# Optimization experiments

Hardware: AMD Instinct MI355X
Metric: run time of the kernel (lower is better)

Reference implementation:

```python
import math
import jax, jax.numpy as jnp
import numpy as np

B, Q, L, H = 32, 40, 1024, 1024
WINDOW_FRAMES, MAX_V_L = 16, 1024
MAX_DELTA = 0.1
NUM_PASSES = 2


def setup_inputs() -> dict:
    key = jax.random.key(0)
    ks = jax.random.split(key, 8)
    init_log_sigma = math.log(WINDOW_FRAMES / (2.0 * MAX_V_L))
    return {
        "pred_spans": jax.random.uniform(ks[0], (B, Q, 2), dtype=jnp.float32),
        "vid_feat": jax.random.normal(ks[1], (B, L, H), dtype=jnp.float32),
        "vid_mask": jnp.ones((B, L), dtype=jnp.float32),
        "txt_rep": jax.random.normal(ks[2], (B, H), dtype=jnp.float32),
        "log_sigma_start": jnp.float32(init_log_sigma),
        "log_sigma_end": jnp.float32(init_log_sigma),
        "sigma_width_scale_start": jnp.float32(0.01),
        "sigma_width_scale_end": jnp.float32(-0.01),
        "txt_proj_w": jax.random.normal(ks[3], (H, 2), dtype=jnp.float32) * 0.02,
        "txt_proj_b": jnp.zeros((2,), dtype=jnp.float32),
        "mlp0_w": jax.random.normal(ks[4], (3 * H, H), dtype=jnp.float32) * (1.0 / math.sqrt(3 * H)),
        "mlp0_b": jnp.zeros((H,), dtype=jnp.float32),
        "mlp1_w": jax.random.normal(ks[5], (H, 2), dtype=jnp.float32) * (1.0 / math.sqrt(H)),
        "mlp1_b": jnp.zeros((2,), dtype=jnp.float32),
    }


def reference(pred_spans, vid_feat, vid_mask, txt_rep,
              log_sigma_start, log_sigma_end,
              sigma_width_scale_start, sigma_width_scale_end,
              txt_proj_w, txt_proj_b, mlp0_w, mlp0_b, mlp1_w, mlp1_b):
    b, q, _ = pred_spans.shape
    l = vid_feat.shape[1]
    # span (center,width) -> (start,end) in [0,1]
    start = jnp.clip(pred_spans[..., 0] - pred_spans[..., 1] / 2, 0.0, 1.0)  # (B,Q)
    end = jnp.clip(pred_spans[..., 0] + pred_spans[..., 1] / 2, 0.0, 1.0)
    t_pos = jnp.linspace(0.0, 1.0, l)  # (L,)
    min_sig = 1.0 / (4.0 * l)
    log_range = math.log(max(float(l) * min_sig * 4.0, 1.0 + 1e-6))
    # semantic sigma offsets (B,2)
    txt_off = jnp.tanh(txt_rep @ txt_proj_w + txt_proj_b) * (0.5 * log_range)
    txt_off_s, txt_off_e = txt_off[:, 0:1], txt_off[:, 1:2]  # (B,1)
    txt_expand = jnp.broadcast_to(txt_rep[:, None, :], (b, q, txt_rep.shape[-1]))
    mask = vid_mask[:, None, :]  # (B,1,L)

    def _pool(anchor, sigma):
        # Gaussian soft-attention pooling over frames; anchor,sigma: (B,Q)
        dist2 = ((t_pos[None, None, :] - anchor[:, :, None]) / sigma[:, :, None]) ** 2
        w = jnp.exp(-0.5 * dist2) * mask  # (B,Q,L)
        w = w / jnp.maximum(jnp.sum(w, -1, keepdims=True), 1e-8)
        return jnp.einsum('bql,blh->bqh', w, vid_feat)

    passes = []
    for _ in range(NUM_PASSES):
        width = jnp.maximum(end - start, 1e-6)  # (B,Q)
        sig_s = jnp.maximum(jnp.exp(log_sigma_start + sigma_width_scale_start * width + txt_off_s), min_sig)
        sig_e = jnp.maximum(jnp.exp(log_sigma_end + sigma_width_scale_end * width + txt_off_e), min_sig)
        start_feat = _pool(start, sig_s)
        end_feat = _pool(end, sig_e)
        joint = jnp.concatenate([start_feat, end_feat, txt_expand], axis=-1)  # (B,Q,3H)
        hidden = jax.nn.relu(joint @ mlp0_w + mlp0_b)
        deltas = jnp.tanh(hidden @ mlp1_w + mlp1_b) * MAX_DELTA  # (B,Q,2)
        start = jnp.clip(start + deltas[..., 0], 0.0, 1.0)
        end = jnp.clip(end + deltas[..., 1], 0.0, 1.0)
        center_r = (start + end) / 2.0
        width_r = jnp.maximum(end - start, 1e-6)
        passes.append(jnp.stack([center_r, width_r], axis=-1))
    return passes[-1], jnp.stack(passes, axis=0)
```

## Files before the change

kernel.cpp:

```cpp
#include <hip/hip_runtime.h>

#define B_   32
#define Q_   40
#define L_   1024
#define H_   1024
#define QQ_  80
#define M_   1280
#define K3_  3072
#define JK_  2048

#define OB_W0T   0u
#define OB_WT2   6291456u
#define OB_JOINT 11534336u
#define OB_PART  16777216u
#define OB_TXTB  27262976u
#define OB_TXTP  27328512u
#define OB_MISC  27590656u
#define MS_START 0
#define MS_END   1280
#define MS_TOS   2560
#define MS_TOE   2592

typedef short bf8 __attribute__((ext_vector_type(8)));
typedef float f4  __attribute__((ext_vector_type(4)));

static __device__ __forceinline__ unsigned short f2b(float f) {
    unsigned int x = __float_as_uint(f);
    unsigned int r = x + 0x7FFFu + ((x >> 16) & 1u);
    return (unsigned short)(r >> 16);
}
static __device__ __forceinline__ float b2f16(unsigned short u) {
    return __uint_as_float((unsigned int)u << 16);
}
static __device__ __forceinline__ float blo(unsigned int u) {
    return __uint_as_float(u << 16);
}
static __device__ __forceinline__ float bhi(unsigned int u) {
    return __uint_as_float(u & 0xffff0000u);
}

__global__ __launch_bounds__(256) void k_setup(const float* __restrict__ w0,
                                               unsigned short* __restrict__ w0t,
                                               const float* __restrict__ txt,
                                               const float* __restrict__ pw,
                                               const float* __restrict__ pb,
                                               const float* __restrict__ spans,
                                               unsigned short* __restrict__ txtb,
                                               float* __restrict__ msc) {
    int z = blockIdx.z, tid = threadIdx.x;
    if (z == 3) {
        int flat = blockIdx.x * 16 + blockIdx.y;
        if (flat < B_) {
            int b = flat;
            int h4 = tid * 4;
            float4 tv = *(const float4*)(txt + (size_t)b * H_ + h4);
            float4 pa = *(const float4*)(pw + 2 * h4);
            float4 pc = *(const float4*)(pw + 2 * h4 + 4);
            float s0 = tv.x * pa.x + tv.y * pa.z + tv.z * pc.x + tv.w * pc.z;
            float s1 = tv.x * pa.y + tv.y * pa.w + tv.z * pc.y + tv.w * pc.w;
            ushort4 o;
            o.x = f2b(tv.x); o.y = f2b(tv.y); o.z = f2b(tv.z); o.w = f2b(tv.w);
            *(ushort4*)(txtb + (size_t)b * H_ + h4) = o;
            __shared__ float r0[256], r1[256];
            r0[tid] = s0; r1[tid] = s1; __syncthreads();
            for (int off = 128; off > 0; off >>= 1) {
                if (tid < off) { r0[tid] += r0[tid + off]; r1[tid] += r1[tid + off]; }
                __syncthreads();
            }
            if (tid == 0) {
                const float half_lr = 4.9999975e-07f;
                msc[MS_TOS + b] = tanhf(r0[0] + pb[0]) * half_lr;
                msc[MS_TOE + b] = tanhf(r1[0] + pb[1]) * half_lr;
            }
        } else if (flat < 37) {
            int i = (flat - B_) * 256 + tid;
            if (i < M_) {
                float c = spans[2 * i], w = spans[2 * i + 1];
                msc[MS_START + i] = fminf(fmaxf(c - 0.5f * w, 0.f), 1.f);
                msc[MS_END + i]   = fminf(fmaxf(c + 0.5f * w, 0.f), 1.f);
            }
        }
        return;
    }
    __shared__ float tile[64][69];
    const float* s = w0 + (size_t)z * 1024 * H_;
    unsigned short* d = w0t + (size_t)z * 1024;
    int r0 = blockIdx.x * 64, c0 = blockIdx.y * 64;
    int col4 = (tid & 15) * 4, row = tid >> 4;
    #pragma unroll
    for (int it = 0; it < 4; it++) {
        int r = it * 16 + row;
        float4 v = *(const float4*)(s + (size_t)(r0 + r) * 1024 + c0 + col4);
        *(float4*)(&tile[r][col4]) = v;
    }
    __syncthreads();
    #pragma unroll
    for (int it = 0; it < 2; it++) {
        int slot = it * 256 + tid;
        int c = slot >> 3, chunk = slot & 7;
        int r = chunk * 8;
        uint4 vv;
        vv.x = (unsigned int)f2b(tile[r + 0][c]) | ((unsigned int)f2b(tile[r + 1][c]) << 16);
        vv.y = (unsigned int)f2b(tile[r + 2][c]) | ((unsigned int)f2b(tile[r + 3][c]) << 16);
        vv.z = (unsigned int)f2b(tile[r + 4][c]) | ((unsigned int)f2b(tile[r + 5][c]) << 16);
        vv.w = (unsigned int)f2b(tile[r + 6][c]) | ((unsigned int)f2b(tile[r + 7][c]) << 16);
        *(uint4*)(d + (size_t)(c0 + c) * K3_ + r0 + r) = vv;
    }
}

static __device__ __forceinline__ void weights_body(int m, float s, float e,
                                                    const float* __restrict__ vmask,
                                                    float ls_s, float ls_e,
                                                    float sw_s, float sw_e,
                                                    const float* __restrict__ msc,
                                                    unsigned short* __restrict__ wt2,
                                                    float* r0, float* r1) {
    int b = m / Q_, q = m - b * Q_;
    int tid = threadIdx.x;
    float width = fmaxf(e - s, 1e-6f);
    const float min_sig = 1.0f / (4.0f * (float)L_);
    float sig_s = fmaxf(expf(ls_s + sw_s * width + msc[MS_TOS + b]), min_sig);
    float sig_e = fmaxf(expf(ls_e + sw_e * width + msc[MS_TOE + b]), min_sig);
    float inv_s = 1.0f / sig_s, inv_e = 1.0f / sig_e;

    float wsv[4], wev[4], sumS = 0.f, sumE = 0.f;
    #pragma unroll
    for (int k = 0; k < 4; k++) {
        int l = tid + k * 256;
        float t = (float)l * (1.0f / 1023.0f);
        float mk = vmask[b * L_ + l];
        float ds = (t - s) * inv_s, de = (t - e) * inv_e;
        float a = expf(-0.5f * ds * ds) * mk;
        float c = expf(-0.5f * de * de) * mk;
        wsv[k] = a; wev[k] = c; sumS += a; sumE += c;
    }
    r0[tid] = sumS; r1[tid] = sumE; __syncthreads();
    for (int off = 128; off > 0; off >>= 1) {
        if (tid < off) { r0[tid] += r0[tid + off]; r1[tid] += r1[tid + off]; }
        __syncthreads();
    }
    float iS = 1.0f / fmaxf(r0[0], 1e-8f);
    float iE = 1.0f / fmaxf(r1[0], 1e-8f);
    unsigned short* wq = wt2 + ((size_t)b * QQ_ + q) * L_;
    unsigned short* we = wt2 + ((size_t)b * QQ_ + Q_ + q) * L_;
    #pragma unroll
    for (int k = 0; k < 4; k++) {
        int l = tid + k * 256;
        wq[l] = f2b(wsv[k] * iS);
        we[l] = f2b(wev[k] * iE);
    }
}

__global__ __launch_bounds__(256) void k_stage2(const float* __restrict__ vmask,
                                                const float* __restrict__ p_ls_s,
                                                const float* __restrict__ p_ls_e,
                                                const float* __restrict__ p_sw_s,
                                                const float* __restrict__ p_sw_e,
                                                const float* __restrict__ msc,
                                                unsigned short* __restrict__ wt2,
                                                const unsigned short* __restrict__ txtb,
                                                const unsigned short* __restrict__ w0t,
                                                unsigned short* __restrict__ txtp) {
    int bid = blockIdx.x;
    if (bid < M_) {
        __shared__ float r0[256], r1[256];
        int m = bid;
        weights_body(m, msc[MS_START + m], msc[MS_END + m], vmask,
                     p_ls_s[0], p_ls_e[0], p_sw_s[0], p_sw_e[0], msc, wt2, r0, r1);
        return;
    }
    int t = bid - M_;
    int nIdx = t & 15, mIdx = (t >> 4) & 1, kIdx = t >> 5;
    int wv = threadIdx.x >> 6, lane = threadIdx.x & 63;
    int ml = lane & 15, kg = lane >> 4;
    int mbase = mIdx * 16;
    int nbase = nIdx * 64 + wv * 16;
    int kz = kIdx * 256;
    const unsigned short* ap = txtb + ((size_t)(mbase + ml) * H_ + kz + kg * 8);
    const unsigned short* bp = w0t + ((size_t)(nbase + ml) * K3_ + JK_ + kz + kg * 8);
    f4 acc = (f4){0.f, 0.f, 0.f, 0.f};
    #pragma unroll
    for (int k0 = 0; k0 < 256; k0 += 32) {
        bf8 a = *(const bf8*)(ap + k0);
        bf8 bb = *(const bf8*)(bp + k0);
        acc = __builtin_amdgcn_mfma_f32_16x16x32_bf16(a, bb, acc, 0, 0, 0);
    }
    unsigned short* pp = txtp + (size_t)kIdx * B_ * H_;
    int n = nbase + ml;
    #pragma unroll
    for (int r = 0; r < 4; r++) {
        int m = mbase + kg * 4 + r;
        pp[(size_t)m * H_ + n] = f2b(acc[r]);
    }
}

__global__ __launch_bounds__(512) void k_pool_mfma(const float* __restrict__ vid,
                                                   const unsigned short* __restrict__ wt2,
                                                   unsigned short* __restrict__ joint) {
    int b = blockIdx.x, ht = blockIdx.y;
    int tid = threadIdx.x;
    int wv = tid >> 6, lane = tid & 63;
    int hsub = wv & 3, half = wv >> 2;
    int ml = lane & 15, kg = lane >> 4;
    int h0 = ht * 64;

    __shared__ __align__(16) unsigned short tileT[2][2][64][40];
    __shared__ float cmb[80][68];

    int st = tid & 255;
    int sl = st >> 3;
    int sh8 = (st & 7) * 8;
    const float* vbase = vid + ((size_t)b * L_ + half * 512) * H_ + h0;

    const unsigned short* ap = wt2 + ((size_t)b * QQ_ + ml) * L_ + half * 512 + kg * 8;

    f4 acc[5];
    #pragma unroll
    for (int t = 0; t < 5; t++) acc[t] = (f4){0.f, 0.f, 0.f, 0.f};

    {
        const float* src = vbase + (size_t)sl * H_ + sh8;
        float4 v0 = *(const float4*)(src);
        float4 v1 = *(const float4*)(src + 4);
        unsigned short* dst = &tileT[half][0][0][0];
        dst[(sh8 + 0) * 40 + sl] = f2b(v0.x);
        dst[(sh8 + 1) * 40 + sl] = f2b(v0.y);
        dst[(sh8 + 2) * 40 + sl] = f2b(v0.z);
        dst[(sh8 + 3) * 40 + sl] = f2b(v0.w);
        dst[(sh8 + 4) * 40 + sl] = f2b(v1.x);
        dst[(sh8 + 5) * 40 + sl] = f2b(v1.y);
        dst[(sh8 + 6) * 40 + sl] = f2b(v1.z);
        dst[(sh8 + 7) * 40 + sl] = f2b(v1.w);
    }
    __syncthreads();

    for (int c = 0; c < 16; c++) {
        int buf = c & 1;
        if (c < 15) {
            const float* src = vbase + (size_t)((c + 1) * 32 + sl) * H_ + sh8;
            float4 v0 = *(const float4*)(src);
            float4 v1 = *(const float4*)(src + 4);
            unsigned short* dst = &tileT[half][buf ^ 1][0][0];
            dst[(sh8 + 0) * 40 + sl] = f2b(v0.x);
            dst[(sh8 + 1) * 40 + sl] = f2b(v0.y);
            dst[(sh8 + 2) * 40 + sl] = f2b(v0.z);
            dst[(sh8 + 3) * 40 + sl] = f2b(v0.w);
            dst[(sh8 + 4) * 40 + sl] = f2b(v1.x);
            dst[(sh8 + 5) * 40 + sl] = f2b(v1.y);
            dst[(sh8 + 6) * 40 + sl] = f2b(v1.z);
            dst[(sh8 + 7) * 40 + sl] = f2b(v1.w);
        }
        bf8 bfrag = *(const bf8*)(&tileT[half][buf][hsub * 16 + ml][kg * 8]);
        int l0 = c * 32;
        #pragma unroll
        for (int t = 0; t < 5; t++) {
            bf8 afr = *(const bf8*)(ap + (size_t)t * 16 * L_ + l0);
            acc[t] = __builtin_amdgcn_mfma_f32_16x16x32_bf16(afr, bfrag, acc[t], 0, 0, 0);
        }
        __syncthreads();
    }

    if (half == 1) {
        #pragma unroll
        for (int t = 0; t < 5; t++)
            #pragma unroll
            for (int r = 0; r < 4; r++)
                cmb[t * 16 + kg * 4 + r][hsub * 16 + ml] = acc[t][r];
    }
    __syncthreads();
    if (half == 0) {
        #pragma unroll
        for (int t = 0; t < 5; t++)
            #pragma unroll
            for (int r = 0; r < 4; r++)
                cmb[t * 16 + kg * 4 + r][hsub * 16 + ml] += acc[t][r];
    }
    __syncthreads();
    for (int idx = tid; idx < 640; idx += 512) {
        int qq = idx >> 3, h8 = (idx & 7) * 8;
        const float* cr = &cmb[qq][h8];
        uint4 vv;
        vv.x = (unsigned int)f2b(cr[0]) | ((unsigned int)f2b(cr[1]) << 16);
        vv.y = (unsigned int)f2b(cr[2]) | ((unsigned int)f2b(cr[3]) << 16);
        vv.z = (unsigned int)f2b(cr[4]) | ((unsigned int)f2b(cr[5]) << 16);
        vv.w = (unsigned int)f2b(cr[6]) | ((unsigned int)f2b(cr[7]) << 16);
        int row = b * Q_ + (qq >= Q_ ? qq - Q_ : qq);
        int col = (qq >= Q_ ? H_ : 0) + h0 + h8;
        *(uint4*)(joint + (size_t)row * JK_ + col) = vv;
    }
}

__global__ __launch_bounds__(256) void k_mlp0_mfma(const unsigned short* __restrict__ joint,
                                                   const unsigned short* __restrict__ w0t,
                                                   const unsigned short* __restrict__ txtp,
                                                   unsigned short* __restrict__ part) {
    int wv = threadIdx.x >> 6, lane = threadIdx.x & 63;
    int ml = lane & 15, kg = lane >> 4;
    int mbase = blockIdx.x * 64 + wv * 16;
    int nbase = blockIdx.y * 64;
    int kbase = blockIdx.z * 512;
    const unsigned short* ap = joint + ((size_t)(mbase + ml) * JK_ + kbase + kg * 8);
    const unsigned short* bp = w0t + ((size_t)(nbase + ml) * K3_ + kbase + kg * 8);
    f4 acc[4];
    #pragma unroll
    for (int t = 0; t < 4; t++) acc[t] = (f4){0.f, 0.f, 0.f, 0.f};

    #pragma unroll 4
    for (int k0 = 0; k0 < 512; k0 += 32) {
        bf8 a = *(const bf8*)(ap + k0);
        #pragma unroll
        for (int t = 0; t < 4; t++) {
            bf8 bb = *(const bf8*)(bp + (size_t)t * 16 * K3_ + k0);
            acc[t] = __builtin_amdgcn_mfma_f32_16x16x32_bf16(a, bb, acc[t], 0, 0, 0);
        }
    }
    const unsigned short* tp = txtp + (size_t)blockIdx.z * B_ * H_;
    unsigned short* pp = part + (size_t)blockIdx.z * M_ * H_;
    #pragma unroll
    for (int t = 0; t < 4; t++) {
        int n = nbase + t * 16 + ml;
        #pragma unroll
        for (int r = 0; r < 4; r++) {
            int m = mbase + kg * 4 + r;
            int b = m / Q_;
            float v = acc[t][r] + b2f16(tp[(size_t)b * H_ + n]);
            pp[(size_t)m * H_ + n] = f2b(v);
        }
    }
}

__global__ __launch_bounds__(256) void k_mlp1w(const float* __restrict__ w1,
                                               const float* __restrict__ b0,
                                               const float* __restrict__ b1,
                                               const unsigned short* __restrict__ part,
                                               float* __restrict__ msc,
                                               float* __restrict__ out, int pass,
                                               int do_weights,
                                               const float* __restrict__ vmask,
                                               const float* __restrict__ p_ls_s,
                                               const float* __restrict__ p_ls_e,
                                               const float* __restrict__ p_sw_s,
                                               const float* __restrict__ p_sw_e,
                                               unsigned short* __restrict__ wt2) {
    int m = blockIdx.x, tid = threadIdx.x;
    int k4 = tid * 4;
    float4 bb = *(const float4*)(b0 + k4);
    float h0 = bb.x, h1 = bb.y, h2 = bb.z, h3 = bb.w;
    #pragma unroll
    for (int z = 0; z < 4; z++) {
        uint2 u = *(const uint2*)(part + (size_t)z * M_ * H_ + (size_t)m * H_ + k4);
        h0 += blo(u.x); h1 += bhi(u.x);
        h2 += blo(u.y); h3 += bhi(u.y);
    }
    h0 = fmaxf(h0, 0.f); h1 = fmaxf(h1, 0.f);
    h2 = fmaxf(h2, 0.f); h3 = fmaxf(h3, 0.f);
    float4 wa = *(const float4*)(w1 + 2 * k4);
    float4 wb = *(const float4*)(w1 + 2 * k4 + 4);
    float p0 = h0 * wa.x + h1 * wa.z + h2 * wb.x + h3 * wb.z;
    float p1 = h0 * wa.y + h1 * wa.w + h2 * wb.y + h3 * wb.w;

    __shared__ float r0[256], r1[256];
    __shared__ float sh_s, sh_e;
    r0[tid] = p0; r1[tid] = p1; __syncthreads();
    for (int off = 128; off > 0; off >>= 1) {
        if (tid < off) { r0[tid] += r0[tid + off]; r1[tid] += r1[tid + off]; }
        __syncthreads();
    }
    if (tid == 0) {
        float d0 = tanhf(r0[0] + b1[0]) * 0.1f;
        float d1 = tanhf(r1[0] + b1[1]) * 0.1f;
        float s = fminf(fmaxf(msc[MS_START + m] + d0, 0.f), 1.f);
        float e = fminf(fmaxf(msc[MS_END + m] + d1, 0.f), 1.f);
        msc[MS_START + m] = s;
        msc[MS_END + m] = e;
        sh_s = s; sh_e = e;
        float cen = 0.5f * (s + e);
        float wid = fmaxf(e - s, 1e-6f);
        out[2560 + (size_t)(pass * M_ + m) * 2 + 0] = cen;
        out[2560 + (size_t)(pass * M_ + m) * 2 + 1] = wid;
        if (pass == 1) { out[2 * m + 0] = cen; out[2 * m + 1] = wid; }
    }
    __syncthreads();
    if (do_weights) {
        weights_body(m, sh_s, sh_e, vmask,
                     p_ls_s[0], p_ls_e[0], p_sw_s[0], p_sw_e[0], msc, wt2, r0, r1);
    }
}

extern "C" void kernel_launch(void* const* d_in, const int* in_sizes, int n_in,
                              void* d_out, int out_size, void* d_ws, size_t ws_size,
                              hipStream_t stream) {
    const float* spans = (const float*)d_in[0];
    const float* vid   = (const float*)d_in[1];
    const float* vmask = (const float*)d_in[2];
    const float* txt   = (const float*)d_in[3];
    const float* ls_s  = (const float*)d_in[4];
    const float* ls_e  = (const float*)d_in[5];
    const float* sw_s  = (const float*)d_in[6];
    const float* sw_e  = (const float*)d_in[7];
    const float* pw    = (const float*)d_in[8];
    const float* pb    = (const float*)d_in[9];
    const float* w0    = (const float*)d_in[10];
    const float* b0    = (const float*)d_in[11];
    const float* w1    = (const float*)d_in[12];
    const float* b1    = (const float*)d_in[13];
    char* wsb = (char*)d_ws;
    unsigned short* w0t   = (unsigned short*)(wsb + OB_W0T);
    unsigned short* wt2   = (unsigned short*)(wsb + OB_WT2);
    unsigned short* joint = (unsigned short*)(wsb + OB_JOINT);
    unsigned short* part  = (unsigned short*)(wsb + OB_PART);
    unsigned short* txtb  = (unsigned short*)(wsb + OB_TXTB);
    unsigned short* txtp  = (unsigned short*)(wsb + OB_TXTP);
    float* msc = (float*)(wsb + OB_MISC);
    float* out = (float*)d_out;

    hipLaunchKernelGGL(k_setup, dim3(16, 16, 4), dim3(256), 0, stream,
                       w0, w0t, txt, pw, pb, spans, txtb, msc);
    hipLaunchKernelGGL(k_stage2, dim3(M_ + 128), dim3(256), 0, stream,
                       vmask, ls_s, ls_e, sw_s, sw_e, msc, wt2, txtb, w0t, txtp);
    for (int p = 0; p < 2; p++) {
        hipLaunchKernelGGL(k_pool_mfma, dim3(B_, 16), dim3(512), 0, stream, vid, wt2, joint);
        hipLaunchKernelGGL(k_mlp0_mfma, dim3(20, 16, 4), dim3(256), 0, stream,
                           joint, w0t, txtp, part);
        hipLaunchKernelGGL(k_mlp1w, dim3(M_), dim3(256), 0, stream,
                           w1, b0, b1, part, msc, out, p, (p == 0) ? 1 : 0,
                           vmask, ls_s, ls_e, sw_s, sw_e, wt2);
    }
}
```

Before: 395.8 us.

## Pre-transpose video features to bf16 once and simplify pooling MFMA kernel

Result: slower. 431.4 us (+9.0%).

```diff
diff --git a/kernel.cpp b/kernel.cpp
--- a/kernel.cpp
+++ b/kernel.cpp
@@ -16,6 +16,7 @@
 #define OB_TXTB  27262976u
 #define OB_TXTP  27328512u
 #define OB_MISC  27590656u
+#define OB_VIDT  28311552u
 #define MS_START 0
 #define MS_END   1280
 #define MS_TOS   2560
@@ -37,6 +38,47 @@
 }
 static __device__ __forceinline__ float bhi(unsigned int u) {
     return __uint_as_float(u & 0xffff0000u);
+}
+
+static __device__ __forceinline__ void block_reduce2(float& a, float& b, float* scr) {
+    #pragma unroll
+    for (int off = 32; off > 0; off >>= 1) {
+        a += __shfl_down(a, off);
+        b += __shfl_down(b, off);
+    }
+    int wv = threadIdx.x >> 6, lane = threadIdx.x & 63;
+    __syncthreads();
+    if (lane == 0) { scr[wv] = a; scr[4 + wv] = b; }
+    __syncthreads();
+    a = scr[0] + scr[1] + scr[2] + scr[3];
+    b = scr[4] + scr[5] + scr[6] + scr[7];
+}
+
+static __device__ __forceinline__ void transpose_tile(const float* __restrict__ src,
+                                                      unsigned short* __restrict__ dst,
+                                                      size_t src_ld, size_t dst_ld,
+                                                      int r0, int c0,
+                                                      float (*tile)[69], int tid) {
+    int col4 = (tid & 15) * 4, row = tid >> 4;
+    #pragma unroll
+    for (int it = 0; it < 4; it++) {
+        int r = it * 16 + row;
+        float4 v = *(const float4*)(src + (size_t)(r0 + r) * src_ld + c0 + col4);
+        *(float4*)(&tile[r][col4]) = v;
+    }
+    __syncthreads();
+    #pragma unroll
+    for (int it = 0; it < 2; it++) {
+        int slot = it * 256 + tid;
+        int c = slot >> 3, chunk = slot & 7;
+        int r = chunk * 8;
+        uint4 vv;
+        vv.x = (unsigned int)f2b(tile[r + 0][c]) | ((unsigned int)f2b(tile[r + 1][c]) << 16);
+        vv.y = (unsigned int)f2b(tile[r + 2][c]) | ((unsigned int)f2b(tile[r + 3][c]) << 16);
+        vv.z = (unsigned int)f2b(tile[r + 4][c]) | ((unsigned int)f2b(tile[r + 5][c]) << 16);
+        vv.w = (unsigned int)f2b(tile[r + 6][c]) | ((unsigned int)f2b(tile[r + 7][c]) << 16);
+        *(uint4*)(dst + (size_t)(c0 + c) * dst_ld + r0 + r) = vv;
+    }
 }
 
 __global__ __launch_bounds__(256) void k_setup(const float* __restrict__ w0,
@@ -46,8 +88,11 @@
                                                const float* __restrict__ pb,
                                                const float* __restrict__ spans,
                                                unsigned short* __restrict__ txtb,
-                                               float* __restrict__ msc) {
+                                               float* __restrict__ msc,
+                                               const float* __restrict__ vid,
+                                               unsigned short* __restrict__ vidt) {
     int z = blockIdx.z, tid = threadIdx.x;
+    __shared__ float tile[64][69];
     if (z == 3) {
         int flat = blockIdx.x * 16 + blockIdx.y;
         if (flat < B_) {
@@ -61,16 +106,12 @@
             ushort4 o;
             o.x = f2b(tv.x); o.y = f2b(tv.y); o.z = f2b(tv.z); o.w = f2b(tv.w);
             *(ushort4*)(txtb + (size_t)b * H_ + h4) = o;
-            __shared__ float r0[256], r1[256];
-            r0[tid] = s0; r1[tid] = s1; __syncthreads();
-            for (int off = 128; off > 0; off >>= 1) {
-                if (tid < off) { r0[tid] += r0[tid + off]; r1[tid] += r1[tid + off]; }
-                __syncthreads();
-            }
+            __shared__ float scr[8];
+            block_reduce2(s0, s1, scr);
             if (tid == 0) {
                 const float half_lr = 4.9999975e-07f;
-                msc[MS_TOS + b] = tanhf(r0[0] + pb[0]) * half_lr;
-                msc[MS_TOE + b] = tanhf(r1[0] + pb[1]) * half_lr;
+                msc[MS_TOS + b] = tanhf(s0 + pb[0]) * half_lr;
+                msc[MS_TOE + b] = tanhf(s1 + pb[1]) * half_lr;
             }
         } else if (flat < 37) {
             int i = (flat - B_) * 256 + tid;
@@ -82,30 +123,14 @@
         }
         return;
     }
-    __shared__ float tile[64][69];
-    const float* s = w0 + (size_t)z * 1024 * H_;
-    unsigned short* d = w0t + (size_t)z * 1024;
-    int r0 = blockIdx.x * 64, c0 = blockIdx.y * 64;
-    int col4 = (tid & 15) * 4, row = tid >> 4;
-    #pragma unroll
-    for (int it = 0; it < 4; it++) {
-        int r = it * 16 + row;
-        float4 v = *(const float4*)(s + (size_t)(r0 + r) * 1024 + c0 + col4);
-        *(float4*)(&tile[r][col4]) = v;
-    }
-    __syncthreads();
-    #pragma unroll
-    for (int it = 0; it < 2; it++) {
-        int slot = it * 256 + tid;
-        int c = slot >> 3, chunk = slot & 7;
-        int r = chunk * 8;
-        uint4 vv;
-        vv.x = (unsigned int)f2b(tile[r + 0][c]) | ((unsigned int)f2b(tile[r + 1][c]) << 16);
-        vv.y = (unsigned int)f2b(tile[r + 2][c]) | ((unsigned int)f2b(tile[r + 3][c]) << 16);
-        vv.z = (unsigned int)f2b(tile[r + 4][c]) | ((unsigned int)f2b(tile[r + 5][c]) << 16);
-        vv.w = (unsigned int)f2b(tile[r + 6][c]) | ((unsigned int)f2b(tile[r + 7][c]) << 16);
-        *(uint4*)(d + (size_t)(c0 + c) * K3_ + r0 + r) = vv;
-    }
+    if (z < 3) {
+        transpose_tile(w0 + (size_t)z * 1024 * H_, w0t + (size_t)z * 1024,
+                       H_, K3_, blockIdx.x * 64, blockIdx.y * 64, tile, tid);
+        return;
+    }
+    int b = z - 4;
+    transpose_tile(vid + (size_t)b * L_ * H_, vidt + (size_t)b * H_ * L_,
+                   H_, L_, blockIdx.x * 64, blockIdx.y * 64, tile, tid);
 }
 
 static __device__ __forceinline__ void weights_body(int m, float s, float e,
@@ -114,7 +139,7 @@
                                                     float sw_s, float sw_e,
                                                     const float* __restrict__ msc,
                                                     unsigned short* __restrict__ wt2,
-                                                    float* r0, float* r1) {
+                                                    float* scr) {
     int b = m / Q_, q = m - b * Q_;
     int tid = threadIdx.x;
     float width = fmaxf(e - s, 1e-6f);
@@ -134,13 +159,9 @@
         float c = expf(-0.5f * de * de) * mk;
         wsv[k] = a; wev[k] = c; sumS += a; sumE += c;
     }
-    r0[tid] = sumS; r1[tid] = sumE; __syncthreads();
-    for (int off = 128; off > 0; off >>= 1) {
-        if (tid < off) { r0[tid] += r0[tid + off]; r1[tid] += r1[tid + off]; }
-        __syncthreads();
-    }
-    float iS = 1.0f / fmaxf(r0[0], 1e-8f);
-    float iE = 1.0f / fmaxf(r1[0], 1e-8f);
+    block_reduce2(sumS, sumE, scr);
+    float iS = 1.0f / fmaxf(sumS, 1e-8f);
+    float iE = 1.0f / fmaxf(sumE, 1e-8f);
     unsigned short* wq = wt2 + ((size_t)b * QQ_ + q) * L_;
     unsigned short* we = wt2 + ((size_t)b * QQ_ + Q_ + q) * L_;
     #pragma unroll
@@ -163,10 +184,10 @@
                                                 unsigned short* __restrict__ txtp) {
     int bid = blockIdx.x;
     if (bid < M_) {
-        __shared__ float r0[256], r1[256];
+        __shared__ float scr[8];
         int m = bid;
         weights_body(m, msc[MS_START + m], msc[MS_END + m], vmask,
-                     p_ls_s[0], p_ls_e[0], p_sw_s[0], p_sw_e[0], msc, wt2, r0, r1);
+                     p_ls_s[0], p_ls_e[0], p_sw_s[0], p_sw_e[0], msc, wt2, scr);
         return;
     }
     int t = bid - M_;
@@ -194,99 +215,40 @@
     }
 }
 
-__global__ __launch_bounds__(512) void k_pool_mfma(const float* __restrict__ vid,
+__global__ __launch_bounds__(256) void k_pool_mfma(const unsigned short* __restrict__ vidt,
                                                    const unsigned short* __restrict__ wt2,
                                                    unsigned short* __restrict__ joint) {
     int b = blockIdx.x, ht = blockIdx.y;
-    int tid = threadIdx.x;
-    int wv = tid >> 6, lane = tid & 63;
-    int hsub = wv & 3, half = wv >> 2;
+    int wv = threadIdx.x >> 6, lane = threadIdx.x & 63;
     int ml = lane & 15, kg = lane >> 4;
-    int h0 = ht * 64;
-
-    __shared__ __align__(16) unsigned short tileT[2][2][64][40];
-    __shared__ float cmb[80][68];
-
-    int st = tid & 255;
-    int sl = st >> 3;
-    int sh8 = (st & 7) * 8;
-    const float* vbase = vid + ((size_t)b * L_ + half * 512) * H_ + h0;
-
-    const unsigned short* ap = wt2 + ((size_t)b * QQ_ + ml) * L_ + half * 512 + kg * 8;
+    int nbase = ht * 64 + wv * 16;
+
+    const unsigned short* ap = wt2 + ((size_t)b * QQ_ + ml) * L_ + kg * 8;
+    const unsigned short* bp = vidt + ((size_t)b * H_ + nbase + ml) * L_ + kg * 8;
 
     f4 acc[5];
     #pragma unroll
     for (int t = 0; t < 5; t++) acc[t] = (f4){0.f, 0.f, 0.f, 0.f};
 
-    {
-        const float* src = vbase + (size_t)sl * H_ + sh8;
-        float4 v0 = *(const float4*)(src);
-        float4 v1 = *(const float4*)(src + 4);
-        unsigned short* dst = &tileT[half][0][0][0];
-        dst[(sh8 + 0) * 40 + sl] = f2b(v0.x);
-        dst[(sh8 + 1) * 40 + sl] = f2b(v0.y);
-        dst[(sh8 + 2) * 40 + sl] = f2b(v0.z);
-        dst[(sh8 + 3) * 40 + sl] = f2b(v0.w);
-        dst[(sh8 + 4) * 40 + sl] = f2b(v1.x);
-        dst[(sh8 + 5) * 40 + sl] = f2b(v1.y);
-        dst[(sh8 + 6) * 40 + sl] = f2b(v1.z);
-        dst[(sh8 + 7) * 40 + sl] = f2b(v1.w);
-    }
-    __syncthreads();
-
-    for (int c = 0; c < 16; c++) {
-        int buf = c & 1;
-        if (c < 15) {
-            const float* src = vbase + (size_t)((c + 1) * 32 + sl) * H_ + sh8;
-            float4 v0 = *(const float4*)(src);
-            float4 v1 = *(const float4*)(src + 4);
-            unsigned short* dst = &tileT[half][buf ^ 1][0][0];
-            dst[(sh8 + 0) * 40 + sl] = f2b(v0.x);
-            dst[(sh8 + 1) * 40 + sl] = f2b(v0.y);
-            dst[(sh8 + 2) * 40 + sl] = f2b(v0.z);
-            dst[(sh8 + 3) * 40 + sl] = f2b(v0.w);
-            dst[(sh8 + 4) * 40 + sl] = f2b(v1.x);
-            dst[(sh8 + 5) * 40 + sl] = f2b(v1.y);
-            dst[(sh8 + 6) * 40 + sl] = f2b(v1.z);
-            dst[(sh8 + 7) * 40 + sl] = f2b(v1.w);
-        }
-        bf8 bfrag = *(const bf8*)(&tileT[half][buf][hsub * 16 + ml][kg * 8]);
-        int l0 = c * 32;
+    #pragma unroll 4
+    for (int k0 = 0; k0 < L_; k0 += 32) {
+        bf8 bb = *(const bf8*)(bp + k0);
         #pragma unroll
         for (int t = 0; t < 5; t++) {
-            bf8 afr = *(const bf8*)(ap + (size_t)t * 16 * L_ + l0);
-            acc[t] = __builtin_amdgcn_mfma_f32_16x16x32_bf16(afr, bfrag, acc[t], 0, 0, 0);
-        }
-        __syncthreads();
-    }
-
-    if (half == 1) {
+            bf8 a = *(const bf8*)(ap + (size_t)t * 16 * L_ + k0);
+            acc[t] = __builtin_amdgcn_mfma_f32_16x16x32_bf16(a, bb, acc[t], 0, 0, 0);
+        }
+    }
+
+    #pragma unroll
+    for (int t = 0; t < 5; t++) {
         #pragma unroll
-        for (int t = 0; t < 5; t++)
-            #pragma unroll
-            for (int r = 0; r < 4; r++)
-                cmb[t * 16 + kg * 4 + r][hsub * 16 + ml] = acc[t][r];
-    }
-    __syncthreads();
-    if (half == 0) {
-        #pragma unroll
-        for (int t = 0; t < 5; t++)
-            #pragma unroll
-            for (int r = 0; r < 4; r++)
-                cmb[t * 16 + kg * 4 + r][hsub * 16 + ml] += acc[t][r];
-    }
-    __syncthreads();
-    for (int idx = tid; idx < 640; idx += 512) {
-        int qq = idx >> 3, h8 = (idx & 7) * 8;
-        const float* cr = &cmb[qq][h8];
-        uint4 vv;
-        vv.x = (unsigned int)f2b(cr[0]) | ((unsigned int)f2b(cr[1]) << 16);
-        vv.y = (unsigned int)f2b(cr[2]) | ((unsigned int)f2b(cr[3]) << 16);
-        vv.z = (unsigned int)f2b(cr[4]) | ((unsigned int)f2b(cr[5]) << 16);
-        vv.w = (unsigned int)f2b(cr[6]) | ((unsigned int)f2b(cr[7]) << 16);
-        int row = b * Q_ + (qq >= Q_ ? qq - Q_ : qq);
-        int col = (qq >= Q_ ? H_ : 0) + h0 + h8;
-        *(uint4*)(joint + (size_t)row * JK_ + col) = vv;
+        for (int r = 0; r < 4; r++) {
+            int qq = t * 16 + kg * 4 + r;
+            int row = b * Q_ + (qq >= Q_ ? qq - Q_ : qq);
+            int col = (qq >= Q_ ? H_ : 0) + nbase + ml;
+            joint[(size_t)row * JK_ + col] = f2b(acc[t][r]);
+        }
     }
 }
 
@@ -359,16 +321,12 @@
     float p0 = h0 * wa.x + h1 * wa.z + h2 * wb.x + h3 * wb.z;
     float p1 = h0 * wa.y + h1 * wa.w + h2 * wb.y + h3 * wb.w;
 
-    __shared__ float r0[256], r1[256];
+    __shared__ float scr[8];
     __shared__ float sh_s, sh_e;
-    r0[tid] = p0; r1[tid] = p1; __syncthreads();
-    for (int off = 128; off > 0; off >>= 1) {
-        if (tid < off) { r0[tid] += r0[tid + off]; r1[tid] += r1[tid + off]; }
-        __syncthreads();
-    }
+    block_reduce2(p0, p1, scr);
     if (tid == 0) {
-        float d0 = tanhf(r0[0] + b1[0]) * 0.1f;
-        float d1 = tanhf(r1[0] + b1[1]) * 0.1f;
+        float d0 = tanhf(p0 + b1[0]) * 0.1f;
+        float d1 = tanhf(p1 + b1[1]) * 0.1f;
         float s = fminf(fmaxf(msc[MS_START + m] + d0, 0.f), 1.f);
         float e = fminf(fmaxf(msc[MS_END + m] + d1, 0.f), 1.f);
         msc[MS_START + m] = s;
@@ -383,7 +341,7 @@
     __syncthreads();
     if (do_weights) {
         weights_body(m, sh_s, sh_e, vmask,
-                     p_ls_s[0], p_ls_e[0], p_sw_s[0], p_sw_e[0], msc, wt2, r0, r1);
+                     p_ls_s[0], p_ls_e[0], p_sw_s[0], p_sw_e[0], msc, wt2, scr);
     }
 }
 
@@ -411,15 +369,16 @@
     unsigned short* part  = (unsigned short*)(wsb + OB_PART);
     unsigned short* txtb  = (unsigned short*)(wsb + OB_TXTB);
     unsigned short* txtp  = (unsigned short*)(wsb + OB_TXTP);
+    unsigned short* vidt  = (unsigned short*)(wsb + OB_VIDT);
     float* msc = (float*)(wsb + OB_MISC);
     float* out = (float*)d_out;
 
-    hipLaunchKernelGGL(k_setup, dim3(16, 16, 4), dim3(256), 0, stream,
-                       w0, w0t, txt, pw, pb, spans, txtb, msc);
+    hipLaunchKernelGGL(k_setup, dim3(16, 16, 36), dim3(256), 0, stream,
+                       w0, w0t, txt, pw, pb, spans, txtb, msc, vid, vidt);
     hipLaunchKernelGGL(k_stage2, dim3(M_ + 128), dim3(256), 0, stream,
                        vmask, ls_s, ls_e, sw_s, sw_e, msc, wt2, txtb, w0t, txtp);
     for (int p = 0; p < 2; p++) {
-        hipLaunchKernelGGL(k_pool_mfma, dim3(B_, 16), dim3(512), 0, stream, vid, wt2, joint);
+        hipLaunchKernelGGL(k_pool_mfma, dim3(B_, 16), dim3(256), 0, stream, vidt, wt2, joint);
         hipLaunchKernelGGL(k_mlp0_mfma, dim3(20, 16, 4), dim3(256), 0, stream,
                            joint, w0t, txtp, part);
         hipLaunchKernelGGL(k_mlp1w, dim3(M_), dim3(256), 0, stream,
```

## Stage pool tiles row-major with transpose LDS reads and LDS-staged weights

Applied to the files above, without the earlier changes.

After: 364.0 us. 8.0% less time.

```diff
diff --git a/kernel.cpp b/kernel.cpp
--- a/kernel.cpp
+++ b/kernel.cpp
@@ -22,6 +22,7 @@
 #define MS_TOE   2592
 
 typedef short bf8 __attribute__((ext_vector_type(8)));
+typedef short bf4 __attribute__((ext_vector_type(4)));
 typedef float f4  __attribute__((ext_vector_type(4)));
 
 static __device__ __forceinline__ unsigned short f2b(float f) {
@@ -29,6 +30,9 @@
     unsigned int r = x + 0x7FFFu + ((x >> 16) & 1u);
     return (unsigned short)(r >> 16);
 }
+static __device__ __forceinline__ unsigned int pk2(float lo, float hi) {
+    return (unsigned int)f2b(lo) | ((unsigned int)f2b(hi) << 16);
+}
 static __device__ __forceinline__ float b2f16(unsigned short u) {
     return __uint_as_float((unsigned int)u << 16);
 }
@@ -37,6 +41,20 @@
 }
 static __device__ __forceinline__ float bhi(unsigned int u) {
     return __uint_as_float(u & 0xffff0000u);
+}
+
+static __device__ __forceinline__ void block_reduce2(float& a, float& b, float* scr) {
+    #pragma unroll
+    for (int off = 32; off > 0; off >>= 1) {
+        a += __shfl_down(a, off);
+        b += __shfl_down(b, off);
+    }
+    int wv = threadIdx.x >> 6, lane = threadIdx.x & 63;
+    __syncthreads();
+    if (lane == 0) { scr[wv] = a; scr[4 + wv] = b; }
+    __syncthreads();
+    a = scr[0] + scr[1] + scr[2] + scr[3];
+    b = scr[4] + scr[5] + scr[6] + scr[7];
 }
 
 __global__ __launch_bounds__(256) void k_setup(const float* __restrict__ w0,
@@ -61,16 +79,12 @@
             ushort4 o;
             o.x = f2b(tv.x); o.y = f2b(tv.y); o.z = f2b(tv.z); o.w = f2b(tv.w);
             *(ushort4*)(txtb + (size_t)b * H_ + h4) = o;
-            __shared__ float r0[256], r1[256];
-            r0[tid] = s0; r1[tid] = s1; __syncthreads();
-            for (int off = 128; off > 0; off >>= 1) {
-                if (tid < off) { r0[tid] += r0[tid + off]; r1[tid] += r1[tid + off]; }
-                __syncthreads();
-            }
+            __shared__ float scr[8];
+            block_reduce2(s0, s1, scr);
             if (tid == 0) {
                 const float half_lr = 4.9999975e-07f;
-                msc[MS_TOS + b] = tanhf(r0[0] + pb[0]) * half_lr;
-                msc[MS_TOE + b] = tanhf(r1[0] + pb[1]) * half_lr;
+                msc[MS_TOS + b] = tanhf(s0 + pb[0]) * half_lr;
+                msc[MS_TOE + b] = tanhf(s1 + pb[1]) * half_lr;
             }
         } else if (flat < 37) {
             int i = (flat - B_) * 256 + tid;
@@ -114,7 +128,7 @@
                                                     float sw_s, float sw_e,
                                                     const float* __restrict__ msc,
                                                     unsigned short* __restrict__ wt2,
-                                                    float* r0, float* r1) {
+                                                    float* scr) {
     int b = m / Q_, q = m - b * Q_;
     int tid = threadIdx.x;
     float width = fmaxf(e - s, 1e-6f);
@@ -134,13 +148,9 @@
         float c = expf(-0.5f * de * de) * mk;
         wsv[k] = a; wev[k] = c; sumS += a; sumE += c;
     }
-    r0[tid] = sumS; r1[tid] = sumE; __syncthreads();
-    for (int off = 128; off > 0; off >>= 1) {
-        if (tid < off) { r0[tid] += r0[tid + off]; r1[tid] += r1[tid + off]; }
-        __syncthreads();
-    }
-    float iS = 1.0f / fmaxf(r0[0], 1e-8f);
-    float iE = 1.0f / fmaxf(r1[0], 1e-8f);
+    block_reduce2(sumS, sumE, scr);
+    float iS = 1.0f / fmaxf(sumS, 1e-8f);
+    float iE = 1.0f / fmaxf(sumE, 1e-8f);
     unsigned short* wq = wt2 + ((size_t)b * QQ_ + q) * L_;
     unsigned short* we = wt2 + ((size_t)b * QQ_ + Q_ + q) * L_;
     #pragma unroll
@@ -163,10 +173,10 @@
                                                 unsigned short* __restrict__ txtp) {
     int bid = blockIdx.x;
     if (bid < M_) {
-        __shared__ float r0[256], r1[256];
+        __shared__ float scr[8];
         int m = bid;
         weights_body(m, msc[MS_START + m], msc[MS_END + m], vmask,
-                     p_ls_s[0], p_ls_e[0], p_sw_s[0], p_sw_e[0], msc, wt2, r0, r1);
+                     p_ls_s[0], p_ls_e[0], p_sw_s[0], p_sw_e[0], msc, wt2, scr);
         return;
     }
     int t = bid - M_;
@@ -204,57 +214,65 @@
     int ml = lane & 15, kg = lane >> 4;
     int h0 = ht * 64;
 
-    __shared__ __align__(16) unsigned short tileT[2][2][64][40];
+    __shared__ __align__(16) unsigned short tb[2][2][2048];
+    __shared__ __align__(16) unsigned short ta[2][2][80 * 40];
     __shared__ float cmb[80][68];
 
     int st = tid & 255;
     int sl = st >> 3;
     int sh8 = (st & 7) * 8;
+    int b_off = ((((sh8 >> 4) * 2 + ((sl >> 2) & 1)) * 4 + (sl >> 3)) * 4 + (sl & 3)) * 16
+                + (sh8 & 15);
     const float* vbase = vid + ((size_t)b * L_ + half * 512) * H_ + h0;
-
-    const unsigned short* ap = wt2 + ((size_t)b * QQ_ + ml) * L_ + half * 512 + kg * 8;
+    const unsigned short* awsrc = wt2 + (size_t)b * QQ_ * L_ + half * 512;
 
     f4 acc[5];
     #pragma unroll
     for (int t = 0; t < 5; t++) acc[t] = (f4){0.f, 0.f, 0.f, 0.f};
 
-    {
-        const float* src = vbase + (size_t)sl * H_ + sh8;
+    auto stage = [&](int c, int buf) {
+        const float* src = vbase + (size_t)(c * 32 + sl) * H_ + sh8;
         float4 v0 = *(const float4*)(src);
         float4 v1 = *(const float4*)(src + 4);
-        unsigned short* dst = &tileT[half][0][0][0];
-        dst[(sh8 + 0) * 40 + sl] = f2b(v0.x);
-        dst[(sh8 + 1) * 40 + sl] = f2b(v0.y);
-        dst[(sh8 + 2) * 40 + sl] = f2b(v0.z);
-        dst[(sh8 + 3) * 40 + sl] = f2b(v0.w);
-        dst[(sh8 + 4) * 40 + sl] = f2b(v1.x);
-        dst[(sh8 + 5) * 40 + sl] = f2b(v1.y);
-        dst[(sh8 + 6) * 40 + sl] = f2b(v1.z);
-        dst[(sh8 + 7) * 40 + sl] = f2b(v1.w);
-    }
+        uint4 w;
+        w.x = pk2(v0.x, v0.y);
+        w.y = pk2(v0.z, v0.w);
+        w.z = pk2(v1.x, v1.y);
+        w.w = pk2(v1.z, v1.w);
+        *(uint4*)(&tb[half][buf][b_off]) = w;
+        {
+            int row = st >> 2, seg = (st & 3) * 8;
+            uint4 av = *(const uint4*)(awsrc + (size_t)row * L_ + c * 32 + seg);
+            *(uint4*)(&ta[half][buf][row * 40 + seg]) = av;
+        }
+        if (st < 64) {
+            int i = st + 256;
+            int row = i >> 2, seg = (i & 3) * 8;
+            uint4 av = *(const uint4*)(awsrc + (size_t)row * L_ + c * 32 + seg);
+            *(uint4*)(&ta[half][buf][row * 40 + seg]) = av;
+        }
+    };
+
+    stage(0, 0);
     __syncthreads();
 
     for (int c = 0; c < 16; c++) {
         int buf = c & 1;
-        if (c < 15) {
-            const float* src = vbase + (size_t)((c + 1) * 32 + sl) * H_ + sh8;
-            float4 v0 = *(const float4*)(src);
-            float4 v1 = *(const float4*)(src + 4);
-            unsigned short* dst = &tileT[half][buf ^ 1][0][0];
-            dst[(sh8 + 0) * 40 + sl] = f2b(v0.x);
-            dst[(sh8 + 1) * 40 + sl] = f2b(v0.y);
-            dst[(sh8 + 2) * 40 + sl] = f2b(v0.z);
-            dst[(sh8 + 3) * 40 + sl] = f2b(v0.w);
-            dst[(sh8 + 4) * 40 + sl] = f2b(v1.x);
-            dst[(sh8 + 5) * 40 + sl] = f2b(v1.y);
-            dst[(sh8 + 6) * 40 + sl] = f2b(v1.z);
-            dst[(sh8 + 7) * 40 + sl] = f2b(v1.w);
-        }
-        bf8 bfrag = *(const bf8*)(&tileT[half][buf][hsub * 16 + ml][kg * 8]);
-        int l0 = c * 32;
+        if (c < 15) stage(c + 1, buf ^ 1);
+
+        unsigned trb = (unsigned)(uintptr_t)(&tb[half][buf][0]) + hsub * 1024 + lane * 8;
+        bf4 lo, hi;
+        asm volatile("ds_read_b64_tr_b16 %0, %2\n\t"
+                     "ds_read_b64_tr_b16 %1, %2 offset:512\n\t"
+                     "s_waitcnt lgkmcnt(0)"
+                     : "=v"(lo), "=v"(hi)
+                     : "v"(trb));
+        __builtin_amdgcn_sched_barrier(0);
+        bf8 bfrag = __builtin_shufflevector(lo, hi, 0, 1, 2, 3, 4, 5, 6, 7);
+
         #pragma unroll
         for (int t = 0; t < 5; t++) {
-            bf8 afr = *(const bf8*)(ap + (size_t)t * 16 * L_ + l0);
+            bf8 afr = *(const bf8*)(&ta[half][buf][(t * 16 + ml) * 40 + kg * 8]);
             acc[t] = __builtin_amdgcn_mfma_f32_16x16x32_bf16(afr, bfrag, acc[t], 0, 0, 0);
         }
         __syncthreads();
@@ -280,10 +298,10 @@
         int qq = idx >> 3, h8 = (idx & 7) * 8;
         const float* cr = &cmb[qq][h8];
         uint4 vv;
-        vv.x = (unsigned int)f2b(cr[0]) | ((unsigned int)f2b(cr[1]) << 16);
-        vv.y = (unsigned int)f2b(cr[2]) | ((unsigned int)f2b(cr[3]) << 16);
-        vv.z = (unsigned int)f2b(cr[4]) | ((unsigned int)f2b(cr[5]) << 16);
-        vv.w = (unsigned int)f2b(cr[6]) | ((unsigned int)f2b(cr[7]) << 16);
+        vv.x = pk2(cr[0], cr[1]);
+        vv.y = pk2(cr[2], cr[3]);
+        vv.z = pk2(cr[4], cr[5]);
+        vv.w = pk2(cr[6], cr[7]);
         int row = b * Q_ + (qq >= Q_ ? qq - Q_ : qq);
         int col = (qq >= Q_ ? H_ : 0) + h0 + h8;
         *(uint4*)(joint + (size_t)row * JK_ + col) = vv;
@@ -359,16 +377,12 @@
     float p0 = h0 * wa.x + h1 * wa.z + h2 * wb.x + h3 * wb.z;
     float p1 = h0 * wa.y + h1 * wa.w + h2 * wb.y + h3 * wb.w;
 
-    __shared__ float r0[256], r1[256];
+    __shared__ float scr[8];
     __shared__ float sh_s, sh_e;
-    r0[tid] = p0; r1[tid] = p1; __syncthreads();
-    for (int off = 128; off > 0; off >>= 1) {
-        if (tid < off) { r0[tid] += r0[tid + off]; r1[tid] += r1[tid + off]; }
-        __syncthreads();
-    }
+    block_reduce2(p0, p1, scr);
     if (tid == 0) {
-        float d0 = tanhf(r0[0] + b1[0]) * 0.1f;
-        float d1 = tanhf(r1[0] + b1[1]) * 0.1f;
+        float d0 = tanhf(p0 + b1[0]) * 0.1f;
+        float d1 = tanhf(p1 + b1[1]) * 0.1f;
         float s = fminf(fmaxf(msc[MS_START + m] + d0, 0.f), 1.f);
         float e = fminf(fmaxf(msc[MS_END + m] + d1, 0.f), 1.f);
         msc[MS_START + m] = s;
@@ -383,7 +397,7 @@
     __syncthreads();
     if (do_weights) {
         weights_body(m, sh_s, sh_e, vmask,
-                     p_ls_s[0], p_ls_e[0], p_sw_s[0], p_sw_e[0], msc, wt2, r0, r1);
+                     p_ls_s[0], p_ls_e[0], p_sw_s[0], p_sw_e[0], msc, wt2, scr);
     }
 }
 
```
